# Performance work log

Hardware: AMD Instinct MI355X
Metric: run time of the kernel (lower is better)

The kernel has to match this reference:

```python
import jax, jax.numpy as jnp
import numpy as np

S, I, H = 4096, 2048, 2048


def setup_inputs() -> dict:
    key = jax.random.key(0)
    ks = jax.random.split(key, 7)
    k = 1.0 / np.sqrt(H)  # torch LSTMCell init range (values don't affect math shape)
    x = jax.random.normal(ks[0], (S, I), dtype=jnp.float32)
    W_ih = jax.random.uniform(ks[1], (4 * H, I), minval=-k, maxval=k, dtype=jnp.float32)
    W_hh = jax.random.uniform(ks[2], (4 * H, H), minval=-k, maxval=k, dtype=jnp.float32)
    b_ih = jax.random.uniform(ks[3], (4 * H,), minval=-k, maxval=k, dtype=jnp.float32)
    b_hh = jax.random.uniform(ks[4], (4 * H,), minval=-k, maxval=k, dtype=jnp.float32)
    xav = np.sqrt(2.0 / (1 + H))  # xavier_normal_ std for a (1, H) tensor
    h0 = jax.random.normal(ks[5], (1, H), dtype=jnp.float32) * xav
    c0 = jax.random.normal(ks[6], (1, H), dtype=jnp.float32) * xav
    return {"x": x, "W_ih": W_ih, "W_hh": W_hh, "b_ih": b_ih, "b_hh": b_hh, "h0": h0, "c0": c0}


def reference(x, W_ih, W_hh, b_ih, b_hh, h0, c0):
    # Precompute input contribution for all timesteps in one big GEMM: (S, 4H)
    x_gates = x @ W_ih.T + b_ih + b_hh
    W_hh_T = W_hh.T  # (H, 4H)

    def step(carry, xg_t):
        h, c = carry  # each (H,)
        gates = xg_t + h @ W_hh_T  # (4H,)
        i, f, g, o = jnp.split(gates, 4)
        i = jax.nn.sigmoid(i)
        f = jax.nn.sigmoid(f)
        g = jnp.tanh(g)
        o = jax.nn.sigmoid(o)
        c_new = f * c + i * g
        h_new = o * jnp.tanh(c_new)
        return (h_new, c_new), h_new

    _, hs = jax.lax.scan(step, (h0[0], c0[0]), x_gates)
    return hs[:, None, :]  # (S, 1, H) matching torch.stack of (1, H) states
```

## Files before the change

kernel.cpp:

```cpp
#include <hip/hip_runtime.h>
#include <hip/hip_bf16.h>

#define S_LEN 4096
#define IDIM  2048
#define HDIM  2048
#define G4    8192
#define NB    256
#define TPB   512

typedef __attribute__((ext_vector_type(8))) short     bf16x8;
typedef __attribute__((ext_vector_type(4))) float     f32x4;

__device__ __forceinline__ unsigned short f2bf(float f) {
  unsigned u = __float_as_uint(f);
  unsigned r = (u + 0x7FFFu + ((u >> 16) & 1u)) >> 16;
  return (unsigned short)r;
}
__device__ __forceinline__ float bf2f(unsigned short h) {
  return __uint_as_float(((unsigned)h) << 16);
}
__device__ __forceinline__ unsigned long long pack_rec(float h, unsigned tag) {
  return (unsigned long long)__float_as_uint(h) | ((unsigned long long)tag << 32);
}

#define BM 128
#define BKK 32
#define LDK 40

__global__ __launch_bounds__(256) void gemm_xg_mfma(
    const float* __restrict__ x, const float* __restrict__ Wih,
    const float* __restrict__ bih, const float* __restrict__ bhh,
    unsigned short* __restrict__ xg) {
  __shared__ unsigned short As[BM][LDK];
  __shared__ unsigned short Bs[BM][LDK];

  const int t = threadIdx.x;
  const int lane = t & 63, wid = t >> 6;
  const int wr = wid >> 1, wc = wid & 1;

  int bid = ((int)blockIdx.x & 7) * 256 + ((int)blockIdx.x >> 3);
  const int s0 = (bid >> 6) * BM;
  const int j0 = (bid & 63) * BM;

  f32x4 acc[4][4] = {};

  float bias[4];
#pragma unroll
  for (int n = 0; n < 4; ++n) {
    const int col = j0 + wc * 64 + n * 16 + (lane & 15);
    bias[n] = bih[col] + bhh[col];
  }

  for (int k0 = 0; k0 < IDIM; k0 += BKK) {
    float4 va[4], vb[4];
#pragma unroll
    for (int u = 0; u < 4; ++u) {
      const int f = t + 256 * u;
      const int row = f >> 3, kc = (f & 7) * 4;
      va[u] = *(const float4*)&x  [(size_t)(s0 + row) * IDIM + k0 + kc];
      vb[u] = *(const float4*)&Wih[(size_t)(j0 + row) * IDIM + k0 + kc];
    }
    __syncthreads();
#pragma unroll
    for (int u = 0; u < 4; ++u) {
      const int f = t + 256 * u;
      const int row = f >> 3, kc = (f & 7) * 4;
      ushort4 pa, pb;
      pa.x = f2bf(va[u].x); pa.y = f2bf(va[u].y);
      pa.z = f2bf(va[u].z); pa.w = f2bf(va[u].w);
      pb.x = f2bf(vb[u].x); pb.y = f2bf(vb[u].y);
      pb.z = f2bf(vb[u].z); pb.w = f2bf(vb[u].w);
      *(ushort4*)&As[row][kc] = pa;
      *(ushort4*)&Bs[row][kc] = pb;
    }
    __syncthreads();

    const int fr = lane & 15, koff = (lane >> 4) * 8;
    bf16x8 a[4], bfr[4];
#pragma unroll
    for (int m = 0; m < 4; ++m)
      a[m] = *(const bf16x8*)&As[wr * 64 + m * 16 + fr][koff];
#pragma unroll
    for (int n = 0; n < 4; ++n)
      bfr[n] = *(const bf16x8*)&Bs[wc * 64 + n * 16 + fr][koff];
#pragma unroll
    for (int m = 0; m < 4; ++m)
#pragma unroll
      for (int n = 0; n < 4; ++n)
        acc[m][n] = __builtin_amdgcn_mfma_f32_16x16x32_bf16(
            a[m], bfr[n], acc[m][n], 0, 0, 0);
  }

#pragma unroll
  for (int m = 0; m < 4; ++m) {
    const int row0 = s0 + wr * 64 + m * 16 + (lane >> 4) * 4;
#pragma unroll
    for (int n = 0; n < 4; ++n) {
      const int col = j0 + wc * 64 + n * 16 + (lane & 15);
#pragma unroll
      for (int r = 0; r < 4; ++r)
        xg[(size_t)(row0 + r) * G4 + col] = f2bf(acc[m][n][r] + bias[n]);
    }
  }
}

__global__ __launch_bounds__(TPB, 2) void lstm_scan(
    const unsigned short* __restrict__ xg, const float* __restrict__ Whh,
    const float* __restrict__ h0, const float* __restrict__ c0,
    float* __restrict__ out, unsigned long long* __restrict__ rec) {
  __shared__ float h_sh[2][2176];

  const int b = blockIdx.x, t = threadIdx.x;
  const int lane = t & 63, wid = t >> 6;
  const int j = b * 8 + wid;

  float w4[4][32];
#pragma unroll
  for (int g = 0; g < 4; ++g) {
    const float* wp = Whh + ((size_t)g * HDIM + j) * HDIM + lane * 32;
#pragma unroll
    for (int i = 0; i < 8; ++i) {
      const float4 v = *(const float4*)(wp + i * 4);
      w4[g][i*4+0] = v.x; w4[g][i*4+1] = v.y;
      w4[g][i*4+2] = v.z; w4[g][i*4+3] = v.w;
    }
  }
  float c_reg = (lane == 0) ? c0[j] : 0.f;
  const int hbase = lane * 32 + ((lane >> 1) << 2);

  for (int ts = 0; ts < S_LEN; ++ts) {
    const int buf = ts & 1;
    float xgv = 0.f;
    if (lane < 4)
      xgv = bf2f(xg[(size_t)ts * G4 + (size_t)lane * HDIM + j]);

    if (ts == 0) {
#pragma unroll
      for (int kk = 0; kk < 4; ++kk) {
        const int idx = t + kk * 512;
        h_sh[0][idx + ((idx >> 6) << 2)] = h0[idx];
      }
    } else {
      const unsigned want = (unsigned)ts;
      const unsigned long long* slot = rec + (size_t)buf * HDIM;
      unsigned long long r0 = 0, r1 = 0, r2 = 0, r3 = 0;
      int d0 = 0, d1 = 0, d2 = 0, d3 = 0;
      for (;;) {
        if (!d0) { r0 = __hip_atomic_load(slot + t,        __ATOMIC_RELAXED, __HIP_MEMORY_SCOPE_AGENT); d0 = ((unsigned)(r0 >> 32) == want); }
        if (!d1) { r1 = __hip_atomic_load(slot + t + 512,  __ATOMIC_RELAXED, __HIP_MEMORY_SCOPE_AGENT); d1 = ((unsigned)(r1 >> 32) == want); }
        if (!d2) { r2 = __hip_atomic_load(slot + t + 1024, __ATOMIC_RELAXED, __HIP_MEMORY_SCOPE_AGENT); d2 = ((unsigned)(r2 >> 32) == want); }
        if (!d3) { r3 = __hip_atomic_load(slot + t + 1536, __ATOMIC_RELAXED, __HIP_MEMORY_SCOPE_AGENT); d3 = ((unsigned)(r3 >> 32) == want); }
        if (d0 & d1 & d2 & d3) break;
        __builtin_amdgcn_s_sleep(1);
      }
      const int i0 = t, i1 = t + 512, i2 = t + 1024, i3 = t + 1536;
      h_sh[buf][i0 + ((i0 >> 6) << 2)] = __uint_as_float((unsigned)r0);
      h_sh[buf][i1 + ((i1 >> 6) << 2)] = __uint_as_float((unsigned)r1);
      h_sh[buf][i2 + ((i2 >> 6) << 2)] = __uint_as_float((unsigned)r2);
      h_sh[buf][i3 + ((i3 >> 6) << 2)] = __uint_as_float((unsigned)r3);
    }
    __syncthreads();

    float a0 = 0.f, a1 = 0.f, a2 = 0.f, a3 = 0.f;
    const float4* h4 = (const float4*)&h_sh[buf][hbase];
#pragma unroll
    for (int i = 0; i < 8; ++i) {
      const float4 hv = h4[i];
      a0 = fmaf(w4[0][i*4+0], hv.x, a0); a0 = fmaf(w4[0][i*4+1], hv.y, a0);
      a0 = fmaf(w4[0][i*4+2], hv.z, a0); a0 = fmaf(w4[0][i*4+3], hv.w, a0);
      a1 = fmaf(w4[1][i*4+0], hv.x, a1); a1 = fmaf(w4[1][i*4+1], hv.y, a1);
      a1 = fmaf(w4[1][i*4+2], hv.z, a1); a1 = fmaf(w4[1][i*4+3], hv.w, a1);
      a2 = fmaf(w4[2][i*4+0], hv.x, a2); a2 = fmaf(w4[2][i*4+1], hv.y, a2);
      a2 = fmaf(w4[2][i*4+2], hv.z, a2); a2 = fmaf(w4[2][i*4+3], hv.w, a2);
      a3 = fmaf(w4[3][i*4+0], hv.x, a3); a3 = fmaf(w4[3][i*4+1], hv.y, a3);
      a3 = fmaf(w4[3][i*4+2], hv.z, a3); a3 = fmaf(w4[3][i*4+3], hv.w, a3);
    }
#pragma unroll
    for (int m = 1; m < 64; m <<= 1) {
      a0 += __shfl_xor(a0, m);
      a1 += __shfl_xor(a1, m);
      a2 += __shfl_xor(a2, m);
      a3 += __shfl_xor(a3, m);
    }
    float sv = (lane == 0) ? a0 : (lane == 1) ? a1 : (lane == 2) ? a2 : a3;
    sv += xgv;
    const float av = (lane == 2) ? tanhf(sv) : 1.f / (1.f + __expf(-sv));
    const float iv = __shfl(av, 0);
    const float fv = __shfl(av, 1);
    const float gv = __shfl(av, 2);
    const float ov = __shfl(av, 3);
    if (lane == 0) {
      c_reg = fmaf(fv, c_reg, iv * gv);
      const float hn = ov * tanhf(c_reg);
      __hip_atomic_store(&rec[(size_t)(buf ^ 1) * HDIM + j],
                         pack_rec(hn, (unsigned)(ts + 1)),
                         __ATOMIC_RELAXED, __HIP_MEMORY_SCOPE_AGENT);
      out[(size_t)ts * HDIM + j] = hn;
    }
  }
}

extern "C" void kernel_launch(void* const* d_in, const int* in_sizes, int n_in,
                              void* d_out, int out_size, void* d_ws, size_t ws_size,
                              hipStream_t stream) {
  const float* x   = (const float*)d_in[0];
  const float* Wih = (const float*)d_in[1];
  const float* Whh = (const float*)d_in[2];
  const float* bih = (const float*)d_in[3];
  const float* bhh = (const float*)d_in[4];
  const float* h0  = (const float*)d_in[5];
  const float* c0  = (const float*)d_in[6];
  float* out = (float*)d_out;

  unsigned long long* rec = (unsigned long long*)d_ws;
  unsigned short* xg = (unsigned short*)((char*)d_ws + 32768);

  hipMemsetAsync(rec, 0, 2 * HDIM * sizeof(unsigned long long), stream);

  gemm_xg_mfma<<<dim3(2048), 256, 0, stream>>>(x, Wih, bih, bhh, xg);

  void* args[] = {(void*)&xg, (void*)&Whh, (void*)&h0,
                  (void*)&c0, (void*)&out, (void*)&rec};
  hipLaunchCooperativeKernel((void*)lstm_scan, dim3(NB), dim3(TPB),
                             args, 0, stream);
}
```

Measured before the change: 12.78 ms.

## Replace per-element tagged h records with per-block flags and out buffer reads

Each step no longer polls 2048 tagged 64-bit records. Wave 0 now polls 256 per-block step counters, then all threads read the previous h directly from the output buffer with 64-bit atomic loads. This cuts the polling traffic per step, but adds an extra block-wide barrier before the flag publish and relies on relaxed ordering between the out store and the flag store. That ordering may allow stale h reads, since no release/acquire fence is used.

```diff
diff --git a/kernel.cpp b/kernel.cpp
--- a/kernel.cpp
+++ b/kernel.cpp
@@ -18,9 +18,6 @@
 }
 __device__ __forceinline__ float bf2f(unsigned short h) {
   return __uint_as_float(((unsigned)h) << 16);
-}
-__device__ __forceinline__ unsigned long long pack_rec(float h, unsigned tag) {
-  return (unsigned long long)__float_as_uint(h) | ((unsigned long long)tag << 32);
 }
 
 #define BM 128
@@ -107,8 +104,8 @@
 __global__ __launch_bounds__(TPB, 2) void lstm_scan(
     const unsigned short* __restrict__ xg, const float* __restrict__ Whh,
     const float* __restrict__ h0, const float* __restrict__ c0,
-    float* __restrict__ out, unsigned long long* __restrict__ rec) {
-  __shared__ float h_sh[2][2176];
+    float* __restrict__ out, unsigned* __restrict__ flags) {
+  __shared__ __align__(16) float h_sh[2][2176];
 
   const int b = blockIdx.x, t = threadIdx.x;
   const int lane = t & 63, wid = t >> 6;
@@ -140,26 +137,33 @@
         const int idx = t + kk * 512;
         h_sh[0][idx + ((idx >> 6) << 2)] = h0[idx];
       }
+      __syncthreads();
     } else {
-      const unsigned want = (unsigned)ts;
-      const unsigned long long* slot = rec + (size_t)buf * HDIM;
-      unsigned long long r0 = 0, r1 = 0, r2 = 0, r3 = 0;
-      int d0 = 0, d1 = 0, d2 = 0, d3 = 0;
-      for (;;) {
-        if (!d0) { r0 = __hip_atomic_load(slot + t,        __ATOMIC_RELAXED, __HIP_MEMORY_SCOPE_AGENT); d0 = ((unsigned)(r0 >> 32) == want); }
-        if (!d1) { r1 = __hip_atomic_load(slot + t + 512,  __ATOMIC_RELAXED, __HIP_MEMORY_SCOPE_AGENT); d1 = ((unsigned)(r1 >> 32) == want); }
-        if (!d2) { r2 = __hip_atomic_load(slot + t + 1024, __ATOMIC_RELAXED, __HIP_MEMORY_SCOPE_AGENT); d2 = ((unsigned)(r2 >> 32) == want); }
-        if (!d3) { r3 = __hip_atomic_load(slot + t + 1536, __ATOMIC_RELAXED, __HIP_MEMORY_SCOPE_AGENT); d3 = ((unsigned)(r3 >> 32) == want); }
-        if (d0 & d1 & d2 & d3) break;
-        __builtin_amdgcn_s_sleep(1);
+      if (wid == 0) {
+        const unsigned want = (unsigned)ts;
+        unsigned f0 = 0, f1 = 0, f2 = 0, f3 = 0;
+        for (;;) {
+          if (f0 < want) f0 = __hip_atomic_load(&flags[lane],       __ATOMIC_RELAXED, __HIP_MEMORY_SCOPE_AGENT);
+          if (f1 < want) f1 = __hip_atomic_load(&flags[lane +  64], __ATOMIC_RELAXED, __HIP_MEMORY_SCOPE_AGENT);
+          if (f2 < want) f2 = __hip_atomic_load(&flags[lane + 128], __ATOMIC_RELAXED, __HIP_MEMORY_SCOPE_AGENT);
+          if (f3 < want) f3 = __hip_atomic_load(&flags[lane + 192], __ATOMIC_RELAXED, __HIP_MEMORY_SCOPE_AGENT);
+          if (f0 >= want && f1 >= want && f2 >= want && f3 >= want) break;
+          __builtin_amdgcn_s_sleep(1);
+        }
       }
-      const int i0 = t, i1 = t + 512, i2 = t + 1024, i3 = t + 1536;
-      h_sh[buf][i0 + ((i0 >> 6) << 2)] = __uint_as_float((unsigned)r0);
-      h_sh[buf][i1 + ((i1 >> 6) << 2)] = __uint_as_float((unsigned)r1);
-      h_sh[buf][i2 + ((i2 >> 6) << 2)] = __uint_as_float((unsigned)r2);
-      h_sh[buf][i3 + ((i3 >> 6) << 2)] = __uint_as_float((unsigned)r3);
-    }
-    __syncthreads();
+      __syncthreads();
+      const float* src = out + (size_t)(ts - 1) * HDIM;
+      const unsigned long long r0 = __hip_atomic_load(
+          (const unsigned long long*)(src) + t,       __ATOMIC_RELAXED, __HIP_MEMORY_SCOPE_AGENT);
+      const unsigned long long r1 = __hip_atomic_load(
+          (const unsigned long long*)(src) + t + 512, __ATOMIC_RELAXED, __HIP_MEMORY_SCOPE_AGENT);
+      const int i0 = t * 2, i1 = t * 2 + 1024;
+      h_sh[buf][i0     + ((i0 >> 6) << 2)] = __uint_as_float((unsigned)(r0));
+      h_sh[buf][i0 + 1 + ((i0 >> 6) << 2)] = __uint_as_float((unsigned)(r0 >> 32));
+      h_sh[buf][i1     + ((i1 >> 6) << 2)] = __uint_as_float((unsigned)(r1));
+      h_sh[buf][i1 + 1 + ((i1 >> 6) << 2)] = __uint_as_float((unsigned)(r1 >> 32));
+      __syncthreads();
+    }
 
     float a0 = 0.f, a1 = 0.f, a2 = 0.f, a3 = 0.f;
     const float4* h4 = (const float4*)&h_sh[buf][hbase];
@@ -192,11 +196,13 @@
     if (lane == 0) {
       c_reg = fmaf(fv, c_reg, iv * gv);
       const float hn = ov * tanhf(c_reg);
-      __hip_atomic_store(&rec[(size_t)(buf ^ 1) * HDIM + j],
-                         pack_rec(hn, (unsigned)(ts + 1)),
+      __hip_atomic_store(&out[(size_t)ts * HDIM + j], hn,
                          __ATOMIC_RELAXED, __HIP_MEMORY_SCOPE_AGENT);
-      out[(size_t)ts * HDIM + j] = hn;
-    }
+    }
+    __syncthreads();
+    if (t == 0)
+      __hip_atomic_store(&flags[b], (unsigned)(ts + 1),
+                         __ATOMIC_RELAXED, __HIP_MEMORY_SCOPE_AGENT);
   }
 }
 
@@ -212,15 +218,15 @@
   const float* c0  = (const float*)d_in[6];
   float* out = (float*)d_out;
 
-  unsigned long long* rec = (unsigned long long*)d_ws;
+  unsigned* flags = (unsigned*)d_ws;
   unsigned short* xg = (unsigned short*)((char*)d_ws + 32768);
 
-  hipMemsetAsync(rec, 0, 2 * HDIM * sizeof(unsigned long long), stream);
+  hipMemsetAsync(flags, 0, NB * sizeof(unsigned), stream);
 
   gemm_xg_mfma<<<dim3(2048), 256, 0, stream>>>(x, Wih, bih, bhh, xg);
 
   void* args[] = {(void*)&xg, (void*)&Whh, (void*)&h0,
-                  (void*)&c0, (void*)&out, (void*)&rec};
+                  (void*)&c0, (void*)&out, (void*)&flags};
   hipLaunchCooperativeKernel((void*)lstm_scan, dim3(NB), dim3(TPB),
                              args, 0, stream);
 }
```

After: 11.62 ms. -9.1%, faster.

## Use output buffer with NaN sentinel as recurrent flag channel and packed FMA

Applied to the files above, without the earlier changes.

Replaces the tagged 64-bit h-exchange buffer with polling directly on the output array, which is prefilled with a quiet-NaN sentinel by a new kernel. Each thread now polls two 64-bit words, each holding two h values, instead of four tagged words, and the redundant separate output store is dropped. The dot product switches to v_pk_fma_f32 on interleaved weight layout with an unpadded single shared buffer. It adds a full-output fill pass and relies on a real h never equaling the sentinel bit pattern.

```diff
diff --git a/kernel.cpp b/kernel.cpp
--- a/kernel.cpp
+++ b/kernel.cpp
@@ -7,9 +7,14 @@
 #define G4    8192
 #define NB    256
 #define TPB   512
-
-typedef __attribute__((ext_vector_type(8))) short     bf16x8;
-typedef __attribute__((ext_vector_type(4))) float     f32x4;
+#define SENT  0x7FC00000u
+
+typedef __attribute__((ext_vector_type(2))) float  f32x2;
+typedef __attribute__((ext_vector_type(4))) float  f32x4;
+typedef __attribute__((ext_vector_type(8))) short  bf16x8;
+
+#define PKFMA(acc, w, h) \
+  asm("v_pk_fma_f32 %0, %1, %2, %0" : "+v"(acc) : "v"(w), "v"(h))
 
 __device__ __forceinline__ unsigned short f2bf(float f) {
   unsigned u = __float_as_uint(f);
@@ -19,8 +24,13 @@
 __device__ __forceinline__ float bf2f(unsigned short h) {
   return __uint_as_float(((unsigned)h) << 16);
 }
-__device__ __forceinline__ unsigned long long pack_rec(float h, unsigned tag) {
-  return (unsigned long long)__float_as_uint(h) | ((unsigned long long)tag << 32);
+
+__global__ __launch_bounds__(256) void fill_sentinel(unsigned long long* p) {
+  const unsigned long long v =
+      ((unsigned long long)SENT << 32) | (unsigned long long)SENT;
+  const int n = S_LEN * HDIM / 2;
+  for (int i = blockIdx.x * 256 + threadIdx.x; i < n; i += gridDim.x * 256)
+    __hip_atomic_store(p + i, v, __ATOMIC_RELAXED, __HIP_MEMORY_SCOPE_AGENT);
 }
 
 #define BM 128
@@ -107,74 +117,75 @@
 __global__ __launch_bounds__(TPB, 2) void lstm_scan(
     const unsigned short* __restrict__ xg, const float* __restrict__ Whh,
     const float* __restrict__ h0, const float* __restrict__ c0,
-    float* __restrict__ out, unsigned long long* __restrict__ rec) {
-  __shared__ float h_sh[2][2176];
+    float* __restrict__ out) {
+  __shared__ __align__(16) float h_sh[HDIM];
 
   const int b = blockIdx.x, t = threadIdx.x;
   const int lane = t & 63, wid = t >> 6;
   const int j = b * 8 + wid;
 
-  float w4[4][32];
+  f32x2 w2[4][16];
 #pragma unroll
   for (int g = 0; g < 4; ++g) {
-    const float* wp = Whh + ((size_t)g * HDIM + j) * HDIM + lane * 32;
+    const float* wp = Whh + ((size_t)g * HDIM + j) * HDIM + lane * 4;
 #pragma unroll
     for (int i = 0; i < 8; ++i) {
-      const float4 v = *(const float4*)(wp + i * 4);
-      w4[g][i*4+0] = v.x; w4[g][i*4+1] = v.y;
-      w4[g][i*4+2] = v.z; w4[g][i*4+3] = v.w;
+      const float4 v = *(const float4*)(wp + i * 256);
+      w2[g][i * 2 + 0] = f32x2{v.x, v.y};
+      w2[g][i * 2 + 1] = f32x2{v.z, v.w};
     }
   }
   float c_reg = (lane == 0) ? c0[j] : 0.f;
-  const int hbase = lane * 32 + ((lane >> 1) << 2);
 
   for (int ts = 0; ts < S_LEN; ++ts) {
-    const int buf = ts & 1;
     float xgv = 0.f;
     if (lane < 4)
       xgv = bf2f(xg[(size_t)ts * G4 + (size_t)lane * HDIM + j]);
 
     if (ts == 0) {
-#pragma unroll
-      for (int kk = 0; kk < 4; ++kk) {
-        const int idx = t + kk * 512;
-        h_sh[0][idx + ((idx >> 6) << 2)] = h0[idx];
-      }
+      h_sh[2*t]        = h0[2*t];
+      h_sh[2*t + 1]    = h0[2*t + 1];
+      h_sh[2*t + 1024] = h0[2*t + 1024];
+      h_sh[2*t + 1025] = h0[2*t + 1025];
     } else {
-      const unsigned want = (unsigned)ts;
-      const unsigned long long* slot = rec + (size_t)buf * HDIM;
-      unsigned long long r0 = 0, r1 = 0, r2 = 0, r3 = 0;
-      int d0 = 0, d1 = 0, d2 = 0, d3 = 0;
+      const unsigned long long* src =
+          (const unsigned long long*)(out + (size_t)(ts - 1) * HDIM);
+      unsigned long long r0 = 0, r1 = 0;
+      int d0 = 0, d1 = 0;
       for (;;) {
-        if (!d0) { r0 = __hip_atomic_load(slot + t,        __ATOMIC_RELAXED, __HIP_MEMORY_SCOPE_AGENT); d0 = ((unsigned)(r0 >> 32) == want); }
-        if (!d1) { r1 = __hip_atomic_load(slot + t + 512,  __ATOMIC_RELAXED, __HIP_MEMORY_SCOPE_AGENT); d1 = ((unsigned)(r1 >> 32) == want); }
-        if (!d2) { r2 = __hip_atomic_load(slot + t + 1024, __ATOMIC_RELAXED, __HIP_MEMORY_SCOPE_AGENT); d2 = ((unsigned)(r2 >> 32) == want); }
-        if (!d3) { r3 = __hip_atomic_load(slot + t + 1536, __ATOMIC_RELAXED, __HIP_MEMORY_SCOPE_AGENT); d3 = ((unsigned)(r3 >> 32) == want); }
-        if (d0 & d1 & d2 & d3) break;
+        if (!d0) {
+          r0 = __hip_atomic_load(src + t, __ATOMIC_RELAXED,
+                                 __HIP_MEMORY_SCOPE_AGENT);
+          d0 = ((unsigned)r0 != SENT) & ((unsigned)(r0 >> 32) != SENT);
+        }
+        if (!d1) {
+          r1 = __hip_atomic_load(src + t + 512, __ATOMIC_RELAXED,
+                                 __HIP_MEMORY_SCOPE_AGENT);
+          d1 = ((unsigned)r1 != SENT) & ((unsigned)(r1 >> 32) != SENT);
+        }
+        if (d0 & d1) break;
         __builtin_amdgcn_s_sleep(1);
       }
-      const int i0 = t, i1 = t + 512, i2 = t + 1024, i3 = t + 1536;
-      h_sh[buf][i0 + ((i0 >> 6) << 2)] = __uint_as_float((unsigned)r0);
-      h_sh[buf][i1 + ((i1 >> 6) << 2)] = __uint_as_float((unsigned)r1);
-      h_sh[buf][i2 + ((i2 >> 6) << 2)] = __uint_as_float((unsigned)r2);
-      h_sh[buf][i3 + ((i3 >> 6) << 2)] = __uint_as_float((unsigned)r3);
+      h_sh[2*t]        = __uint_as_float((unsigned)r0);
+      h_sh[2*t + 1]    = __uint_as_float((unsigned)(r0 >> 32));
+      h_sh[2*t + 1024] = __uint_as_float((unsigned)r1);
+      h_sh[2*t + 1025] = __uint_as_float((unsigned)(r1 >> 32));
     }
     __syncthreads();
 
-    float a0 = 0.f, a1 = 0.f, a2 = 0.f, a3 = 0.f;
-    const float4* h4 = (const float4*)&h_sh[buf][hbase];
+    f32x2 A0 = {0.f, 0.f}, A1 = {0.f, 0.f}, A2 = {0.f, 0.f}, A3 = {0.f, 0.f};
+    const f32x4* h4 = (const f32x4*)&h_sh[lane * 4];
 #pragma unroll
     for (int i = 0; i < 8; ++i) {
-      const float4 hv = h4[i];
-      a0 = fmaf(w4[0][i*4+0], hv.x, a0); a0 = fmaf(w4[0][i*4+1], hv.y, a0);
-      a0 = fmaf(w4[0][i*4+2], hv.z, a0); a0 = fmaf(w4[0][i*4+3], hv.w, a0);
-      a1 = fmaf(w4[1][i*4+0], hv.x, a1); a1 = fmaf(w4[1][i*4+1], hv.y, a1);
-      a1 = fmaf(w4[1][i*4+2], hv.z, a1); a1 = fmaf(w4[1][i*4+3], hv.w, a1);
-      a2 = fmaf(w4[2][i*4+0], hv.x, a2); a2 = fmaf(w4[2][i*4+1], hv.y, a2);
-      a2 = fmaf(w4[2][i*4+2], hv.z, a2); a2 = fmaf(w4[2][i*4+3], hv.w, a2);
-      a3 = fmaf(w4[3][i*4+0], hv.x, a3); a3 = fmaf(w4[3][i*4+1], hv.y, a3);
-      a3 = fmaf(w4[3][i*4+2], hv.z, a3); a3 = fmaf(w4[3][i*4+3], hv.w, a3);
-    }
+      const f32x4 hv = h4[i * 64];
+      const f32x2 hlo = {hv.x, hv.y}, hhi = {hv.z, hv.w};
+      PKFMA(A0, w2[0][i*2+0], hlo); PKFMA(A0, w2[0][i*2+1], hhi);
+      PKFMA(A1, w2[1][i*2+0], hlo); PKFMA(A1, w2[1][i*2+1], hhi);
+      PKFMA(A2, w2[2][i*2+0], hlo); PKFMA(A2, w2[2][i*2+1], hhi);
+      PKFMA(A3, w2[3][i*2+0], hlo); PKFMA(A3, w2[3][i*2+1], hhi);
+    }
+    float a0 = A0.x + A0.y, a1 = A1.x + A1.y;
+    float a2 = A2.x + A2.y, a3 = A3.x + A3.y;
 #pragma unroll
     for (int m = 1; m < 64; m <<= 1) {
       a0 += __shfl_xor(a0, m);
@@ -192,10 +203,8 @@
     if (lane == 0) {
       c_reg = fmaf(fv, c_reg, iv * gv);
       const float hn = ov * tanhf(c_reg);
-      __hip_atomic_store(&rec[(size_t)(buf ^ 1) * HDIM + j],
-                         pack_rec(hn, (unsigned)(ts + 1)),
+      __hip_atomic_store(&out[(size_t)ts * HDIM + j], hn,
                          __ATOMIC_RELAXED, __HIP_MEMORY_SCOPE_AGENT);
-      out[(size_t)ts * HDIM + j] = hn;
     }
   }
 }
@@ -212,15 +221,11 @@
   const float* c0  = (const float*)d_in[6];
   float* out = (float*)d_out;
 
-  unsigned long long* rec = (unsigned long long*)d_ws;
-  unsigned short* xg = (unsigned short*)((char*)d_ws + 32768);
-
-  hipMemsetAsync(rec, 0, 2 * HDIM * sizeof(unsigned long long), stream);
-
+  unsigned short* xg = (unsigned short*)d_ws;
+
+  fill_sentinel<<<dim3(2048), 256, 0, stream>>>((unsigned long long*)out);
   gemm_xg_mfma<<<dim3(2048), 256, 0, stream>>>(x, Wih, bih, bhh, xg);
-
-  void* args[] = {(void*)&xg, (void*)&Whh, (void*)&h0,
-                  (void*)&c0, (void*)&out, (void*)&rec};
+  void* args[] = {(void*)&xg, (void*)&Whh, (void*)&h0, (void*)&c0, (void*)&out};
   hipLaunchCooperativeKernel((void*)lstm_scan, dim3(NB), dim3(TPB),
                              args, 0, stream);
 }
```

New measurement: 14.00 ms. 1.1x slower.
